# Optimization experiments

Measured on AMD Instinct MI355X. Metric: run time of the kernel, lower is better.

## Reference

```python
import jax, jax.numpy as jnp
import numpy as np

N_NODES = 25000
N_EDGES = 400000
CHANNELS = 32
EDGE_FEAT_DIM = 8
HIDDEN = 64
NUM_IRREPS = 4  # messages irreps = 2x0e + 2x1o -> 4 irreps, dim 8
AVG_NUM_NEIGHBORS = 16.0


def _mlp(x, W0, W1, W2, W3):
    # e3nn MultiLayerPerceptron: dense layers with 1/sqrt(fan_in) forward
    # normalization, silu on hidden layers, no output activation.
    for W in (W0, W1, W2):
        x = jax.nn.silu(x @ (W / jnp.sqrt(jnp.float32(W.shape[0]))))
    return x @ (W3 / jnp.sqrt(jnp.float32(W3.shape[0])))


def setup_inputs() -> dict:
    key = jax.random.key(0)
    ks = jax.random.split(key, 9)
    node_feats = jax.random.normal(ks[0], (N_NODES, CHANNELS, 4), jnp.float32)
    edge_attrs = jax.random.normal(ks[1], (N_EDGES, 4), jnp.float32)
    edge_feats = jax.random.normal(ks[2], (N_EDGES, EDGE_FEAT_DIM), jnp.float32)
    senders = jax.random.randint(ks[3], (N_EDGES,), 0, N_NODES)
    receivers = jax.random.randint(ks[4], (N_EDGES,), 0, N_NODES)
    W0 = jax.random.normal(ks[5], (EDGE_FEAT_DIM, HIDDEN), jnp.float32)
    W1 = jax.random.normal(ks[6], (HIDDEN, HIDDEN), jnp.float32)
    W2 = jax.random.normal(ks[7], (HIDDEN, HIDDEN), jnp.float32)
    W3 = jax.random.normal(ks[8], (HIDDEN, CHANNELS * NUM_IRREPS), jnp.float32)
    return {"node_feats": node_feats, "edge_attrs": edge_attrs,
            "edge_feats": edge_feats, "senders": senders, "receivers": receivers,
            "W0": W0, "W1": W1, "W2": W2, "W3": W3}


def reference(node_feats, edge_attrs, edge_feats, senders, receivers, W0, W1, W2, W3):
    # Gather sender node features: [E, C, 4] with irreps 0e (dim1) + 1o (dim3)
    x = node_feats[senders]
    s, v = x[..., 0], x[..., 1:4]            # [E,C], [E,C,3]
    a_s = edge_attrs[:, 0]                   # Y_0: [E]
    a_v = edge_attrs[:, 1:4]                 # Y_1: [E,3]

    # CG tensor product filtered to 0e + 1o (e3nn normalization: sqrt(2l3+1)*w3j)
    m0a = s * a_s[:, None]                                   # 0e x 0e -> 0e  [E,C]
    m0b = jnp.einsum('ecd,ed->ec', v, a_v) / jnp.sqrt(3.0)   # 1o x 1o -> 0e  [E,C]
    m1a = s[..., None] * a_v[:, None, :]                     # 0e x 1o -> 1o  [E,C,3]
    m1b = v * a_s[:, None, None]                             # 1o x 0e -> 1o  [E,C,3]

    # Edge MLP gate: [E, C*num_irreps] -> mul_to_axis -> [E, C, num_irreps]
    mix = _mlp(edge_feats, W0, W1, W2, W3).reshape(N_EDGES, CHANNELS, NUM_IRREPS)

    # Elementwise tensor product with 4x0e scalars: per-irrep gating
    out_s = jnp.stack([m0a * mix[..., 0], m0b * mix[..., 1]], axis=-1)          # [E,C,2]
    out_v = jnp.concatenate([m1a * mix[..., 2:3], m1b * mix[..., 3:4]], axis=-1)  # [E,C,6]
    messages = jnp.concatenate([out_s, out_v], axis=-1)                          # [E,C,8]

    # Scatter-add into receivers, then normalize by sqrt(avg_num_neighbors)
    agg = jax.ops.segment_sum(messages, receivers, num_segments=N_NODES)
    return agg / jnp.sqrt(AVG_NUM_NEIGHBORS)
```

## Files before the change

### kernel.cpp

```cpp
#include <hip/hip_runtime.h>
#include <hip/hip_fp16.h>

#define NE 400000
#define NN 25000
#define MAXDEG 56
#define LDS_STRIDE 65

typedef __attribute__((ext_vector_type(8))) _Float16 half8;
typedef __attribute__((ext_vector_type(4))) _Float16 half4;
typedef __attribute__((ext_vector_type(4))) float f32x4;

#define WS_MIX_OFF   0ull
#define WS_SLOTS_OFF 102400000ull
#define WS_CNT_OFF   108000000ull
#define WS_WBUF_OFF  108100000ull
#define WS_NEED      108136864ull

#define WB_L0 0
#define WB_L1 2048
#define WB_L2 6144
#define WB_L3 10240

__device__ __forceinline__ float fast_silu(float x) {
    float e = __expf(-x);
    return x * __builtin_amdgcn_rcpf(1.0f + e);
}

__global__ __launch_bounds__(64) void prep_weights(
    const float* __restrict__ W0, const float* __restrict__ W1,
    const float* __restrict__ W2, const float* __restrict__ W3,
    _Float16* __restrict__ wbuf, int* __restrict__ cnt)
{
    const int f    = blockIdx.x;
    const int lane = threadIdx.x;

    for (int i = f * 64 + lane; i < NN; i += 36 * 64) cnt[i] = 0;

    const int n    = lane & 15;
    const int quad = lane >> 4;

    const float* W; int K, N, kt, nt, fl, base; float scale;
    if (f < 4)       { W = W0; K = 8;  N = 64;  fl = f;      kt = 0;       nt = fl;     scale = 0.35355339059327373f; base = WB_L0; }
    else if (f < 12) { W = W1; K = 64; N = 64;  fl = f - 4;  kt = fl >> 2; nt = fl & 3; scale = 0.125f;   base = WB_L1; }
    else if (f < 20) { W = W2; K = 64; N = 64;  fl = f - 12; kt = fl >> 2; nt = fl & 3; scale = 0.125f;   base = WB_L2; }
    else             { W = W3; K = 64; N = 128; fl = f - 20; kt = fl >> 3; nt = fl & 7; scale = 0.03125f; base = WB_L3; }

    _Float16 v[8];
    #pragma unroll
    for (int j = 0; j < 8; ++j) {
        const int k = kt * 32 + quad * 8 + j;
        const float val = (k < K) ? W[k * N + nt * 16 + n] * scale : 0.0f;
        v[j] = (_Float16)val;
    }
    *(half8*)(wbuf + base + fl * 512 + lane * 8) = *(const half8*)v;
}

#define HS 72
__global__ __launch_bounds__(256) void mlp_build_kernel(
    const float*    __restrict__ edge_feats,
    const int*      __restrict__ receivers,
    const _Float16* __restrict__ wbuf,
    int*            __restrict__ cnt,
    int*            __restrict__ slots,
    _Float16*       __restrict__ mix16)
{
    __shared__ _Float16 H[4 * 2 * 16 * HS];
    const int tid  = threadIdx.x;
    const int wave = tid >> 6;
    const int lane = tid & 63;
    const int col  = lane & 15;
    const int quad = lane >> 4;

    if (tid < 128) {
        const int e = blockIdx.x * 128 + tid;
        const int r = receivers[e];
        const int s = atomicAdd(&cnt[r], 1);
        if (s < MAXDEG) slots[r * MAXDEG + s] = e;
    }

    const int e0 = (blockIdx.x * 4 + wave) * 32;
    _Float16* HA = &H[wave * 2 * 16 * HS];
    _Float16* HB = HA + 16 * HS;
    const half8* wb = (const half8*)wbuf;
    const f32x4 zero4 = {0.f, 0.f, 0.f, 0.f};

    half8 b0A = {0, 0, 0, 0, 0, 0, 0, 0};
    half8 b0B = {0, 0, 0, 0, 0, 0, 0, 0};
    if (quad == 0) {
        const float4* pA = (const float4*)(edge_feats + (size_t)(e0 + col) * 8);
        const float4 xa = pA[0], ya = pA[1];
        b0A[0] = (_Float16)xa.x; b0A[1] = (_Float16)xa.y; b0A[2] = (_Float16)xa.z; b0A[3] = (_Float16)xa.w;
        b0A[4] = (_Float16)ya.x; b0A[5] = (_Float16)ya.y; b0A[6] = (_Float16)ya.z; b0A[7] = (_Float16)ya.w;
        const float4* pB = (const float4*)(edge_feats + (size_t)(e0 + 16 + col) * 8);
        const float4 xb = pB[0], yb = pB[1];
        b0B[0] = (_Float16)xb.x; b0B[1] = (_Float16)xb.y; b0B[2] = (_Float16)xb.z; b0B[3] = (_Float16)xb.w;
        b0B[4] = (_Float16)yb.x; b0B[5] = (_Float16)yb.y; b0B[6] = (_Float16)yb.z; b0B[7] = (_Float16)yb.w;
    }

    #pragma unroll
    for (int nt = 0; nt < 4; ++nt) {
        const half8 w = wb[(WB_L0 / 512 + nt) * 64 + lane];
        f32x4 aA = __builtin_amdgcn_mfma_f32_16x16x32_f16(w, b0A, zero4, 0, 0, 0);
        f32x4 aB = __builtin_amdgcn_mfma_f32_16x16x32_f16(w, b0B, zero4, 0, 0, 0);
        half4 hA, hB;
        #pragma unroll
        for (int r = 0; r < 4; ++r) { hA[r] = (_Float16)fast_silu(aA[r]); hB[r] = (_Float16)fast_silu(aB[r]); }
        *(half4*)&HA[col * HS + nt * 16 + quad * 4] = hA;
        *(half4*)&HB[col * HS + nt * 16 + quad * 4] = hB;
    }

    #pragma unroll
    for (int layer = 0; layer < 2; ++layer) {
        const int wbase = (layer == 0 ? WB_L1 : WB_L2) / 512;
        const half8 bloA = *(const half8*)&HA[col * HS + 0  + quad * 8];
        const half8 bhiA = *(const half8*)&HA[col * HS + 32 + quad * 8];
        const half8 bloB = *(const half8*)&HB[col * HS + 0  + quad * 8];
        const half8 bhiB = *(const half8*)&HB[col * HS + 32 + quad * 8];
        f32x4 aA[4], aB[4];
        #pragma unroll
        for (int nt = 0; nt < 4; ++nt) {
            const half8 wlo = wb[(wbase + 0 + nt) * 64 + lane];
            const half8 whi = wb[(wbase + 4 + nt) * 64 + lane];
            aA[nt] = __builtin_amdgcn_mfma_f32_16x16x32_f16(wlo, bloA, zero4, 0, 0, 0);
            aA[nt] = __builtin_amdgcn_mfma_f32_16x16x32_f16(whi, bhiA, aA[nt], 0, 0, 0);
            aB[nt] = __builtin_amdgcn_mfma_f32_16x16x32_f16(wlo, bloB, zero4, 0, 0, 0);
            aB[nt] = __builtin_amdgcn_mfma_f32_16x16x32_f16(whi, bhiB, aB[nt], 0, 0, 0);
        }
        #pragma unroll
        for (int nt = 0; nt < 4; ++nt) {
            half4 hA, hB;
            #pragma unroll
            for (int r = 0; r < 4; ++r) { hA[r] = (_Float16)fast_silu(aA[nt][r]); hB[r] = (_Float16)fast_silu(aB[nt][r]); }
            *(half4*)&HA[col * HS + nt * 16 + quad * 4] = hA;
            *(half4*)&HB[col * HS + nt * 16 + quad * 4] = hB;
        }
    }

    {
        const half8 bloA = *(const half8*)&HA[col * HS + 0  + quad * 8];
        const half8 bhiA = *(const half8*)&HA[col * HS + 32 + quad * 8];
        const half8 bloB = *(const half8*)&HB[col * HS + 0  + quad * 8];
        const half8 bhiB = *(const half8*)&HB[col * HS + 32 + quad * 8];
        _Float16* mrowA = mix16 + (size_t)(e0 + col) * 128;
        _Float16* mrowB = mix16 + (size_t)(e0 + 16 + col) * 128;
        #pragma unroll
        for (int nt = 0; nt < 8; ++nt) {
            const half8 wlo = wb[(WB_L3 / 512 + 0 + nt) * 64 + lane];
            const half8 whi = wb[(WB_L3 / 512 + 8 + nt) * 64 + lane];
            f32x4 aA = __builtin_amdgcn_mfma_f32_16x16x32_f16(wlo, bloA, zero4, 0, 0, 0);
            aA = __builtin_amdgcn_mfma_f32_16x16x32_f16(whi, bhiA, aA, 0, 0, 0);
            f32x4 aB = __builtin_amdgcn_mfma_f32_16x16x32_f16(wlo, bloB, zero4, 0, 0, 0);
            aB = __builtin_amdgcn_mfma_f32_16x16x32_f16(whi, bhiB, aB, 0, 0, 0);
            half4 hA, hB;
            #pragma unroll
            for (int r = 0; r < 4; ++r) { hA[r] = (_Float16)aA[r]; hB[r] = (_Float16)aB[r]; }
            *(half4*)&mrowA[nt * 16 + quad * 4] = hA;
            *(half4*)&mrowB[nt * 16 + quad * 4] = hB;
        }
    }
}

__global__ __launch_bounds__(64) void gather_kernel(
    const float*    __restrict__ node_feats,
    const float*    __restrict__ edge_attrs,
    const int*      __restrict__ senders,
    const _Float16* __restrict__ mix16,
    const int*      __restrict__ cnt,
    const int*      __restrict__ slots,
    float*          __restrict__ out)
{
    const int n    = blockIdx.x;
    const int lane = threadIdx.x;
    const int g    = lane >> 4;
    const int s    = lane & 15;
    const int c0   = 2 * s;
    const float inv_sqrt3 = 0.5773502691896258f;

    int d = cnt[n];
    if (d > MAXDEG) d = MAXDEG;
    const int* sl = slots + n * MAXDEG;

    float acc[16];
    #pragma unroll
    for (int j = 0; j < 16; ++j) acc[j] = 0.0f;

    #pragma unroll 2
    for (int base = 0; base < d; base += 4) {
        const int  ei  = base + g;
        const bool act = (ei < d);
        const int  eic = act ? ei : 0;
        const int  eid = sl[eic];
        const int  snd = senders[eid];
        const float4 a4v = ((const float4*)edge_attrs)[eid];
        const half8 m8 = *(const half8*)(mix16 + (size_t)eid * 128 + c0 * 4);
        const float4 xA = ((const float4*)(node_feats + (size_t)snd * 128))[c0];
        const float4 xB = ((const float4*)(node_feats + (size_t)snd * 128))[c0 + 1];

        const float z = act ? 1.0f : 0.0f;
        const float as = a4v.x, av0 = a4v.y, av1 = a4v.z, av2 = a4v.w;

        {
            const float m0 = z * (float)m8[0], m1 = z * (float)m8[1];
            const float m2 = z * (float)m8[2], m3 = z * (float)m8[3];
            const float sc = xA.x, v0 = xA.y, v1 = xA.z, v2 = xA.w;
            acc[0] = fmaf(sc * as, m0, acc[0]);
            const float dv = v0 * av0 + v1 * av1 + v2 * av2;
            acc[1] = fmaf(dv * inv_sqrt3, m1, acc[1]);
            acc[2] = fmaf(sc * av0, m2, acc[2]);
            acc[3] = fmaf(sc * av1, m2, acc[3]);
            acc[4] = fmaf(sc * av2, m2, acc[4]);
            acc[5] = fmaf(v0 * as, m3, acc[5]);
            acc[6] = fmaf(v1 * as, m3, acc[6]);
            acc[7] = fmaf(v2 * as, m3, acc[7]);
        }
        {
            const float m0 = z * (float)m8[4], m1 = z * (float)m8[5];
            const float m2 = z * (float)m8[6], m3 = z * (float)m8[7];
            const float sc = xB.x, v0 = xB.y, v1 = xB.z, v2 = xB.w;
            acc[8]  = fmaf(sc * as, m0, acc[8]);
            const float dv = v0 * av0 + v1 * av1 + v2 * av2;
            acc[9]  = fmaf(dv * inv_sqrt3, m1, acc[9]);
            acc[10] = fmaf(sc * av0, m2, acc[10]);
            acc[11] = fmaf(sc * av1, m2, acc[11]);
            acc[12] = fmaf(sc * av2, m2, acc[12]);
            acc[13] = fmaf(v0 * as, m3, acc[13]);
            acc[14] = fmaf(v1 * as, m3, acc[14]);
            acc[15] = fmaf(v2 * as, m3, acc[15]);
        }
    }

    #pragma unroll
    for (int j = 0; j < 16; ++j) {
        acc[j] += __shfl_xor(acc[j], 16, 64);
        acc[j] += __shfl_xor(acc[j], 32, 64);
    }

    if (g == 0) {
        float4* op = (float4*)(out + (size_t)n * 256 + s * 16);
        float4 r0; r0.x = acc[0];  r0.y = acc[1];  r0.z = acc[2];  r0.w = acc[3];
        float4 r1; r1.x = acc[4];  r1.y = acc[5];  r1.z = acc[6];  r1.w = acc[7];
        float4 r2; r2.x = acc[8];  r2.y = acc[9];  r2.z = acc[10]; r2.w = acc[11];
        float4 r3; r3.x = acc[12]; r3.y = acc[13]; r3.z = acc[14]; r3.w = acc[15];
        op[0] = r0; op[1] = r1; op[2] = r2; op[3] = r3;
    }
}

__global__ __launch_bounds__(128) void edge_mp_kernel(
    const float* __restrict__ node_feats, const float* __restrict__ edge_attrs,
    const float* __restrict__ edge_feats, const int* __restrict__ senders,
    const int* __restrict__ receivers, const float* __restrict__ W0,
    const float* __restrict__ W1, const float* __restrict__ W2,
    const float* __restrict__ W3, float* __restrict__ out)
{
    __shared__ float hbuf[128 * LDS_STRIDE];
    const int tid = threadIdx.x;
    const int e   = blockIdx.x * 128 + tid;
    if (e >= NE) return;
    float* hl = &hbuf[tid * LDS_STRIDE];

    float4 ef0 = ((const float4*)edge_feats)[e * 2 + 0];
    float4 ef1 = ((const float4*)edge_feats)[e * 2 + 1];
    float ef[8] = {ef0.x, ef0.y, ef0.z, ef0.w, ef1.x, ef1.y, ef1.z, ef1.w};
    float acc[64];
    #pragma unroll
    for (int i = 0; i < 64; ++i) acc[i] = 0.0f;
    #pragma unroll
    for (int j = 0; j < 8; ++j) {
        const float xj = ef[j];
        const float* wrow = W0 + j * 64;
        #pragma unroll
        for (int i = 0; i < 64; ++i) acc[i] = fmaf(xj, wrow[i], acc[i]);
    }
    {
        const float s0 = 0.35355339059327373f;
        #pragma unroll
        for (int i = 0; i < 64; ++i) hl[i] = fast_silu(acc[i] * s0);
    }
    #pragma unroll
    for (int i = 0; i < 64; ++i) acc[i] = 0.0f;
    #pragma unroll 4
    for (int j = 0; j < 64; ++j) {
        const float xj = hl[j];
        const float* wrow = W1 + j * 64;
        #pragma unroll
        for (int i = 0; i < 64; ++i) acc[i] = fmaf(xj, wrow[i], acc[i]);
    }
    #pragma unroll
    for (int i = 0; i < 64; ++i) hl[i] = fast_silu(acc[i] * 0.125f);
    #pragma unroll
    for (int i = 0; i < 64; ++i) acc[i] = 0.0f;
    #pragma unroll 4
    for (int j = 0; j < 64; ++j) {
        const float xj = hl[j];
        const float* wrow = W2 + j * 64;
        #pragma unroll
        for (int i = 0; i < 64; ++i) acc[i] = fmaf(xj, wrow[i], acc[i]);
    }
    float h2[64];
    #pragma unroll
    for (int i = 0; i < 64; ++i) h2[i] = fast_silu(acc[i] * 0.125f);

    const int snd = senders[e];
    const int rcv = receivers[e];
    const float4 a4 = ((const float4*)edge_attrs)[e];
    const float a_s = a4.x, av0 = a4.y, av1 = a4.z, av2 = a4.w;
    const float4* nf4 = (const float4*)(node_feats + (size_t)snd * 128);
    float* outp = out + (size_t)rcv * 256;
    const float mixscale = 0.03125f;
    const float inv_sqrt3 = 0.5773502691896258f;

    #pragma unroll 2
    for (int c = 0; c < 32; ++c) {
        float m0 = 0.0f, m1 = 0.0f, m2 = 0.0f, m3 = 0.0f;
        const float* wc = W3 + c * 4;
        #pragma unroll
        for (int j = 0; j < 64; ++j) {
            const float hj = h2[j];
            m0 = fmaf(hj, wc[j * 128 + 0], m0);
            m1 = fmaf(hj, wc[j * 128 + 1], m1);
            m2 = fmaf(hj, wc[j * 128 + 2], m2);
            m3 = fmaf(hj, wc[j * 128 + 3], m3);
        }
        m0 *= mixscale; m1 *= mixscale; m2 *= mixscale; m3 *= mixscale;
        const float4 x4 = nf4[c];
        const float s = x4.x, v0 = x4.y, v1 = x4.z, v2 = x4.w;
        float* op = outp + c * 8;
        atomicAdd(op + 0, s * a_s * m0);
        const float dotva = v0 * av0 + v1 * av1 + v2 * av2;
        atomicAdd(op + 1, dotva * inv_sqrt3 * m1);
        atomicAdd(op + 2, s * av0 * m2);
        atomicAdd(op + 3, s * av1 * m2);
        atomicAdd(op + 4, s * av2 * m2);
        atomicAdd(op + 5, v0 * a_s * m3);
        atomicAdd(op + 6, v1 * a_s * m3);
        atomicAdd(op + 7, v2 * a_s * m3);
    }
}

extern "C" void kernel_launch(void* const* d_in, const int* in_sizes, int n_in,
                              void* d_out, int out_size, void* d_ws, size_t ws_size,
                              hipStream_t stream) {
    const float* node_feats = (const float*)d_in[0];
    const float* edge_attrs = (const float*)d_in[1];
    const float* edge_feats = (const float*)d_in[2];
    const int*   senders    = (const int*)d_in[3];
    const int*   receivers  = (const int*)d_in[4];
    const float* W0 = (const float*)d_in[5];
    const float* W1 = (const float*)d_in[6];
    const float* W2 = (const float*)d_in[7];
    const float* W3 = (const float*)d_in[8];
    float* outp = (float*)d_out;

    if (ws_size >= WS_NEED) {
        char* w = (char*)d_ws;
        _Float16* mix16 = (_Float16*)(w + WS_MIX_OFF);
        int*      slots = (int*)(w + WS_SLOTS_OFF);
        int*      cnt   = (int*)(w + WS_CNT_OFF);
        _Float16* wbuf  = (_Float16*)(w + WS_WBUF_OFF);

        hipLaunchKernelGGL(prep_weights, dim3(36), dim3(64), 0, stream,
                           W0, W1, W2, W3, wbuf, cnt);
        hipLaunchKernelGGL(mlp_build_kernel, dim3(NE / 128), dim3(256), 0, stream,
                           edge_feats, receivers, wbuf, cnt, slots, mix16);
        hipLaunchKernelGGL(gather_kernel, dim3(NN), dim3(64), 0, stream,
                           node_feats, edge_attrs, senders, mix16, cnt, slots, outp);
    } else {
        hipMemsetAsync(d_out, 0, (size_t)out_size * sizeof(float), stream);
        hipLaunchKernelGGL(edge_mp_kernel, dim3((NE + 127) / 128), dim3(128), 0, stream,
                           node_feats, edge_attrs, edge_feats, senders, receivers,
                           W0, W1, W2, W3, outp);
    }
}
```

Measured before the change: 217.8 us.

## Widen MLP waves to 64 edges and prefetch slot/sender indices via shuffles

The MLP build kernel now runs 128-thread blocks where each wave processes 64 edges (four 16-edge tiles) instead of 32. Each weight fragment loaded from the workspace is therefore reused across more MFMAs, and all threads take part in the slot-building atomics. The gather kernel loads each node's slot list and sender ids once, one per lane, and broadcasts them with wave shuffles instead of doing dependent global loads every iteration. The cost is higher register pressure in the MLP kernel, which may reduce occupancy.

```diff
diff --git a/kernel.cpp b/kernel.cpp
--- a/kernel.cpp
+++ b/kernel.cpp
@@ -56,7 +56,7 @@
 }
 
 #define HS 72
-__global__ __launch_bounds__(256) void mlp_build_kernel(
+__global__ __launch_bounds__(128, 4) void mlp_build_kernel(
     const float*    __restrict__ edge_feats,
     const int*      __restrict__ receivers,
     const _Float16* __restrict__ wbuf,
@@ -64,98 +64,111 @@
     int*            __restrict__ slots,
     _Float16*       __restrict__ mix16)
 {
-    __shared__ _Float16 H[4 * 2 * 16 * HS];
+    __shared__ _Float16 H[2 * 4 * 16 * HS];
     const int tid  = threadIdx.x;
     const int wave = tid >> 6;
     const int lane = tid & 63;
     const int col  = lane & 15;
     const int quad = lane >> 4;
 
-    if (tid < 128) {
+    {
         const int e = blockIdx.x * 128 + tid;
         const int r = receivers[e];
         const int s = atomicAdd(&cnt[r], 1);
         if (s < MAXDEG) slots[r * MAXDEG + s] = e;
     }
 
-    const int e0 = (blockIdx.x * 4 + wave) * 32;
-    _Float16* HA = &H[wave * 2 * 16 * HS];
-    _Float16* HB = HA + 16 * HS;
+    const int e0 = (blockIdx.x * 2 + wave) * 64;
+    _Float16* HW = &H[wave * 4 * 16 * HS];
     const half8* wb = (const half8*)wbuf;
     const f32x4 zero4 = {0.f, 0.f, 0.f, 0.f};
 
-    half8 b0A = {0, 0, 0, 0, 0, 0, 0, 0};
-    half8 b0B = {0, 0, 0, 0, 0, 0, 0, 0};
+    half8 b0[4];
+    #pragma unroll
+    for (int t = 0; t < 4; ++t) {
+        half8 z = {0, 0, 0, 0, 0, 0, 0, 0};
+        b0[t] = z;
+    }
     if (quad == 0) {
-        const float4* pA = (const float4*)(edge_feats + (size_t)(e0 + col) * 8);
-        const float4 xa = pA[0], ya = pA[1];
-        b0A[0] = (_Float16)xa.x; b0A[1] = (_Float16)xa.y; b0A[2] = (_Float16)xa.z; b0A[3] = (_Float16)xa.w;
-        b0A[4] = (_Float16)ya.x; b0A[5] = (_Float16)ya.y; b0A[6] = (_Float16)ya.z; b0A[7] = (_Float16)ya.w;
-        const float4* pB = (const float4*)(edge_feats + (size_t)(e0 + 16 + col) * 8);
-        const float4 xb = pB[0], yb = pB[1];
-        b0B[0] = (_Float16)xb.x; b0B[1] = (_Float16)xb.y; b0B[2] = (_Float16)xb.z; b0B[3] = (_Float16)xb.w;
-        b0B[4] = (_Float16)yb.x; b0B[5] = (_Float16)yb.y; b0B[6] = (_Float16)yb.z; b0B[7] = (_Float16)yb.w;
+        #pragma unroll
+        for (int t = 0; t < 4; ++t) {
+            const float4* p = (const float4*)(edge_feats + (size_t)(e0 + t * 16 + col) * 8);
+            const float4 x = p[0], y = p[1];
+            b0[t][0] = (_Float16)x.x; b0[t][1] = (_Float16)x.y; b0[t][2] = (_Float16)x.z; b0[t][3] = (_Float16)x.w;
+            b0[t][4] = (_Float16)y.x; b0[t][5] = (_Float16)y.y; b0[t][6] = (_Float16)y.z; b0[t][7] = (_Float16)y.w;
+        }
     }
 
     #pragma unroll
     for (int nt = 0; nt < 4; ++nt) {
         const half8 w = wb[(WB_L0 / 512 + nt) * 64 + lane];
-        f32x4 aA = __builtin_amdgcn_mfma_f32_16x16x32_f16(w, b0A, zero4, 0, 0, 0);
-        f32x4 aB = __builtin_amdgcn_mfma_f32_16x16x32_f16(w, b0B, zero4, 0, 0, 0);
-        half4 hA, hB;
-        #pragma unroll
-        for (int r = 0; r < 4; ++r) { hA[r] = (_Float16)fast_silu(aA[r]); hB[r] = (_Float16)fast_silu(aB[r]); }
-        *(half4*)&HA[col * HS + nt * 16 + quad * 4] = hA;
-        *(half4*)&HB[col * HS + nt * 16 + quad * 4] = hB;
+        f32x4 a[4];
+        #pragma unroll
+        for (int t = 0; t < 4; ++t)
+            a[t] = __builtin_amdgcn_mfma_f32_16x16x32_f16(w, b0[t], zero4, 0, 0, 0);
+        #pragma unroll
+        for (int t = 0; t < 4; ++t) {
+            half4 h;
+            #pragma unroll
+            for (int r = 0; r < 4; ++r) h[r] = (_Float16)fast_silu(a[t][r]);
+            *(half4*)&HW[t * 16 * HS + col * HS + nt * 16 + quad * 4] = h;
+        }
     }
 
     #pragma unroll
     for (int layer = 0; layer < 2; ++layer) {
         const int wbase = (layer == 0 ? WB_L1 : WB_L2) / 512;
-        const half8 bloA = *(const half8*)&HA[col * HS + 0  + quad * 8];
-        const half8 bhiA = *(const half8*)&HA[col * HS + 32 + quad * 8];
-        const half8 bloB = *(const half8*)&HB[col * HS + 0  + quad * 8];
-        const half8 bhiB = *(const half8*)&HB[col * HS + 32 + quad * 8];
-        f32x4 aA[4], aB[4];
+        half8 blo[4], bhi[4];
+        #pragma unroll
+        for (int t = 0; t < 4; ++t) {
+            blo[t] = *(const half8*)&HW[t * 16 * HS + col * HS + 0  + quad * 8];
+            bhi[t] = *(const half8*)&HW[t * 16 * HS + col * HS + 32 + quad * 8];
+        }
         #pragma unroll
         for (int nt = 0; nt < 4; ++nt) {
             const half8 wlo = wb[(wbase + 0 + nt) * 64 + lane];
             const half8 whi = wb[(wbase + 4 + nt) * 64 + lane];
-            aA[nt] = __builtin_amdgcn_mfma_f32_16x16x32_f16(wlo, bloA, zero4, 0, 0, 0);
-            aA[nt] = __builtin_amdgcn_mfma_f32_16x16x32_f16(whi, bhiA, aA[nt], 0, 0, 0);
-            aB[nt] = __builtin_amdgcn_mfma_f32_16x16x32_f16(wlo, bloB, zero4, 0, 0, 0);
-            aB[nt] = __builtin_amdgcn_mfma_f32_16x16x32_f16(whi, bhiB, aB[nt], 0, 0, 0);
-        }
-        #pragma unroll
-        for (int nt = 0; nt < 4; ++nt) {
-            half4 hA, hB;
+            f32x4 a[4];
             #pragma unroll
-            for (int r = 0; r < 4; ++r) { hA[r] = (_Float16)fast_silu(aA[nt][r]); hB[r] = (_Float16)fast_silu(aB[nt][r]); }
-            *(half4*)&HA[col * HS + nt * 16 + quad * 4] = hA;
-            *(half4*)&HB[col * HS + nt * 16 + quad * 4] = hB;
+            for (int t = 0; t < 4; ++t) {
+                a[t] = __builtin_amdgcn_mfma_f32_16x16x32_f16(wlo, blo[t], zero4, 0, 0, 0);
+                a[t] = __builtin_amdgcn_mfma_f32_16x16x32_f16(whi, bhi[t], a[t], 0, 0, 0);
+            }
+            #pragma unroll
+            for (int t = 0; t < 4; ++t) {
+                half4 h;
+                #pragma unroll
+                for (int r = 0; r < 4; ++r) h[r] = (_Float16)fast_silu(a[t][r]);
+                *(half4*)&HW[t * 16 * HS + col * HS + nt * 16 + quad * 4] = h;
+            }
         }
     }
 
     {
-        const half8 bloA = *(const half8*)&HA[col * HS + 0  + quad * 8];
-        const half8 bhiA = *(const half8*)&HA[col * HS + 32 + quad * 8];
-        const half8 bloB = *(const half8*)&HB[col * HS + 0  + quad * 8];
-        const half8 bhiB = *(const half8*)&HB[col * HS + 32 + quad * 8];
-        _Float16* mrowA = mix16 + (size_t)(e0 + col) * 128;
-        _Float16* mrowB = mix16 + (size_t)(e0 + 16 + col) * 128;
+        half8 blo[4], bhi[4];
+        #pragma unroll
+        for (int t = 0; t < 4; ++t) {
+            blo[t] = *(const half8*)&HW[t * 16 * HS + col * HS + 0  + quad * 8];
+            bhi[t] = *(const half8*)&HW[t * 16 * HS + col * HS + 32 + quad * 8];
+        }
+        _Float16* mrow0 = mix16 + (size_t)(e0 + 0 * 16 + col) * 128;
+        _Float16* mrow1 = mix16 + (size_t)(e0 + 1 * 16 + col) * 128;
+        _Float16* mrow2 = mix16 + (size_t)(e0 + 2 * 16 + col) * 128;
+        _Float16* mrow3 = mix16 + (size_t)(e0 + 3 * 16 + col) * 128;
+        _Float16* mrow[4] = {mrow0, mrow1, mrow2, mrow3};
         #pragma unroll
         for (int nt = 0; nt < 8; ++nt) {
             const half8 wlo = wb[(WB_L3 / 512 + 0 + nt) * 64 + lane];
             const half8 whi = wb[(WB_L3 / 512 + 8 + nt) * 64 + lane];
-            f32x4 aA = __builtin_amdgcn_mfma_f32_16x16x32_f16(wlo, bloA, zero4, 0, 0, 0);
-            aA = __builtin_amdgcn_mfma_f32_16x16x32_f16(whi, bhiA, aA, 0, 0, 0);
-            f32x4 aB = __builtin_amdgcn_mfma_f32_16x16x32_f16(wlo, bloB, zero4, 0, 0, 0);
-            aB = __builtin_amdgcn_mfma_f32_16x16x32_f16(whi, bhiB, aB, 0, 0, 0);
-            half4 hA, hB;
             #pragma unroll
-            for (int r = 0; r < 4; ++r) { hA[r] = (_Float16)aA[r]; hB[r] = (_Float16)aB[r]; }
-            *(half4*)&mrowA[nt * 16 + quad * 4] = hA;
-            *(half4*)&mrowB[nt * 16 + quad * 4] = hB;
+            for (int t = 0; t < 4; ++t) {
+                f32x4 a = __builtin_amdgcn_mfma_f32_16x16x32_f16(wlo, blo[t], zero4, 0, 0, 0);
+                a = __builtin_amdgcn_mfma_f32_16x16x32_f16(whi, bhi[t], a, 0, 0, 0);
+                half4 h;
+                #pragma unroll
+                for (int r = 0; r < 4; ++r) h[r] = (_Float16)a[r];
+                *(half4*)&mrow[t][nt * 16 + quad * 4] = h;
+            }
         }
     }
 }
@@ -180,6 +193,11 @@
     if (d > MAXDEG) d = MAXDEG;
     const int* sl = slots + n * MAXDEG;
 
+    const int li    = (lane < MAXDEG) ? lane : (MAXDEG - 1);
+    int eid_l       = sl[li];
+    eid_l           = (lane < d) ? eid_l : 0;
+    const int snd_l = senders[eid_l];
+
     float acc[16];
     #pragma unroll
     for (int j = 0; j < 16; ++j) acc[j] = 0.0f;
@@ -188,9 +206,8 @@
     for (int base = 0; base < d; base += 4) {
         const int  ei  = base + g;
         const bool act = (ei < d);
-        const int  eic = act ? ei : 0;
-        const int  eid = sl[eic];
-        const int  snd = senders[eid];
+        const int  eid = __shfl(eid_l, ei, 64);
+        const int  snd = __shfl(snd_l, ei, 64);
         const float4 a4v = ((const float4*)edge_attrs)[eid];
         const half8 m8 = *(const half8*)(mix16 + (size_t)eid * 128 + c0 * 4);
         const float4 xA = ((const float4*)(node_feats + (size_t)snd * 128))[c0];
@@ -360,7 +377,7 @@
 
         hipLaunchKernelGGL(prep_weights, dim3(36), dim3(64), 0, stream,
                            W0, W1, W2, W3, wbuf, cnt);
-        hipLaunchKernelGGL(mlp_build_kernel, dim3(NE / 128), dim3(256), 0, stream,
+        hipLaunchKernelGGL(mlp_build_kernel, dim3(NE / 128), dim3(128), 0, stream,
                            edge_feats, receivers, wbuf, cnt, slots, mix16);
         hipLaunchKernelGGL(gather_kernel, dim3(NN), dim3(64), 0, stream,
                            node_feats, edge_attrs, senders, mix16, cnt, slots, outp);
```

New measurement: 213.4 us. 1.02x faster.
